# Optimization experiments

Hardware: AMD Instinct MI355X
Metric: run time of the kernel (lower is better)

## Reference

```python
import jax, jax.numpy as jnp
import numpy as np

NUM_E = 50000
EMBED_DIM = 128
HID_DIM = 200
B = 512
N = 50  # candidate_num / history length
ITER_NUM = 3
ALPHA = 0.5
WEIGHT_BASE = 1.0
SQUASH_W = 1.0
SQUASH_EPS = 1e-9
L2_EPS = 1e-12  # torch F.normalize default eps


def setup_inputs() -> dict:
    key = jax.random.key(0)
    k1, k2, k3, k4, k5, k6, k7 = jax.random.split(key, 7)
    idx = jax.random.randint(k1, (B, N), 0, NUM_E)
    times = jax.random.randint(k2, (B, N), 0, 365)
    # embeddings: normal then row-wise L2 normalize (as in init_embeddings)
    emb = jax.random.normal(k3, (NUM_E, EMBED_DIM), dtype=jnp.float32)
    embeddings = emb / jnp.maximum(jnp.linalg.norm(emb, axis=1, keepdims=True), L2_EPS)
    Ws_w = jax.random.normal(k4, (HID_DIM, EMBED_DIM), dtype=jnp.float32) * (2.0 / (HID_DIM + EMBED_DIM)) ** 0.5
    Ws_b = jnp.zeros((HID_DIM,), dtype=jnp.float32)
    mlp_w = jax.random.normal(k5, (NUM_E, HID_DIM), dtype=jnp.float32) * (2.0 / (NUM_E + HID_DIM)) ** 0.5
    mlp_b = jnp.zeros((NUM_E,), dtype=jnp.float32)
    return {"idx": idx, "times": times, "embeddings": embeddings,
            "Ws_w": Ws_w, "Ws_b": Ws_b, "mlp_w": mlp_w, "mlp_b": mlp_b}


def _squash(s):
    # s: [B, H]; squash over last axis (original axis=-2 on [B,1,1,H,1])
    sq = jnp.sum(s * s, axis=-1, keepdims=True)
    scale = sq / (SQUASH_W + sq) / jnp.sqrt(sq + SQUASH_EPS)
    return scale * s


def reference(idx, times, embeddings, Ws_w, Ws_b, mlp_w, mlp_b):
    # gather history embeddings: [B, N, D]
    embeds = embeddings[idx]
    # temporal weighting -> initial routing logits b_ij: [B, N]
    b = (WEIGHT_BASE + 1.0) / (WEIGHT_BASE + times.astype(jnp.float32))
    # Ws linear (dropout is identity at eval): [B, N, H]
    x = jnp.einsum('bnd,hd->bnh', embeds, Ws_w) + Ws_b
    # u_hat: L2-normalized over H
    u_hat = x / jnp.maximum(jnp.linalg.norm(x, axis=-1, keepdims=True), L2_EPS)
    u_det = jax.lax.stop_gradient(u_hat)
    # dynamic routing, fixed ITER_NUM iterations
    for r in range(ITER_NUM):
        c = jax.nn.softmax(b, axis=1) * N            # [B, N]
        s = jnp.einsum('bn,bnh->bh', c, u_hat)       # [B, H]
        v = _squash(s)                               # [B, H]
        if r < ITER_NUM - 1:
            b = b + jnp.einsum('bnh,bh->bn', u_det, v)
    poses, c_ij = v, c                               # [B, H], [B, N]
    # p_ij: scatter-add c_ij per entity id (math of one_hot^T @ c_ij)
    p = jnp.zeros((B, NUM_E), dtype=jnp.float32)
    p = p.at[jnp.arange(B)[:, None], idx].add(c_ij)
    p = jax.nn.softmax(p, axis=1)
    # decoder mlp (reflect=False)
    scores = poses @ mlp_w.T + mlp_b                 # [B, NUM_E]
    sims = jax.nn.softmax(scores, axis=1)
    return jnp.log(ALPHA * p + (1.0 - ALPHA) * sims)
```

## Files before the change

### kernel.cpp

```cpp
#include <hip/hip_runtime.h>
#include <stdint.h>

#define NUM_E 50000
#define EMBED_DIM 128
#define HID_DIM 200
#define BATCH 512
#define NN 50
#define KPAD 224
#define NKT 7
#define NTT2 3136
#define NXB 196
#define PACK_UNITS 784
#define USTRIDE 201
#define EPS 264

typedef short s16x8 __attribute__((ext_vector_type(8)));
typedef float f32x4 __attribute__((ext_vector_type(4)));

__device__ inline unsigned short f2bf(float f) {
  union { float f; unsigned u; } v; v.f = f;
  unsigned r = v.u + 0x7FFF + ((v.u >> 16) & 1);
  return (unsigned short)(r >> 16);
}
__device__ inline float bf2f(unsigned short b) {
  union { unsigned u; float f; } v; v.u = ((unsigned)b) << 16;
  return v.f;
}

__device__ __forceinline__ void gl_lds16(const unsigned short* g, unsigned short* l) {
  __builtin_amdgcn_global_load_lds(
      (const __attribute__((address_space(1))) unsigned int*)g,
      (__attribute__((address_space(3))) unsigned int*)l, 16, 0, 0);
}

__global__ __launch_bounds__(256, 4) void k_score(
    const unsigned short* __restrict__ Ap, const unsigned short* __restrict__ Bp,
    const float* __restrict__ mlp_b, unsigned short* __restrict__ stash,
    float* __restrict__ S_ws)
{
  __shared__ __align__(16) char buf[34816];
  unsigned short (*Bs)[8192] = (unsigned short (*)[8192])buf;
  unsigned short* ep = (unsigned short*)buf;
  float* red = (float*)(buf + 33792);
  const int id = blockIdx.x;
  const int yb = id / 200;
  const int xb = id - yb * 200;
  if (xb >= NXB) return;

  const int tid = threadIdx.x;
  const int w = tid >> 6, lane = tid & 63;
  const int q = lane >> 4, l15 = lane & 15;
  const int mt0 = yb * 4;
  const int m0 = yb * 64;
  const int ntb = xb * 16 + w * 4;

  float bias[4];
  #pragma unroll
  for (int nl = 0; nl < 4; ++nl) {
    const int col = (ntb + nl) * 16 + l15;
    bias[nl] = (col < NUM_E) ? mlp_b[col] : 0.f;
  }
  const unsigned short* apB = Ap + (size_t)mt0 * NKT * 512 + (size_t)lane * 8;
  const unsigned short* bpB = Bp + (size_t)ntb * NKT * 512 + (size_t)lane * 8;

  f32x4 acc[4][4];
  #pragma unroll
  for (int i = 0; i < 4; i++)
    #pragma unroll
    for (int j = 0; j < 4; j++) acc[i][j] = (f32x4){0, 0, 0, 0};

  s16x8 areg[2][4];

  #pragma unroll
  for (int nl = 0; nl < 4; ++nl)
    gl_lds16(bpB + (size_t)nl * NKT * 512, &Bs[0][(w * 4 + nl) * 512]);
  #pragma unroll
  for (int mi = 0; mi < 4; ++mi)
    areg[0][mi] = *(const s16x8*)(apB + (size_t)(mi * NKT) * 512);
  __syncthreads();

  #pragma unroll
  for (int kt = 0; kt < NKT; ++kt) {
    const int cur = kt & 1;
    if (kt < NKT - 1) {
      #pragma unroll
      for (int nl = 0; nl < 4; ++nl)
        gl_lds16(bpB + (size_t)(nl * NKT + kt + 1) * 512,
                 &Bs[cur ^ 1][(w * 4 + nl) * 512]);
      #pragma unroll
      for (int mi = 0; mi < 4; ++mi)
        areg[cur ^ 1][mi] = *(const s16x8*)(apB + (size_t)(mi * NKT + kt + 1) * 512);
    }
    s16x8 bfr[4];
    #pragma unroll
    for (int nl = 0; nl < 4; ++nl)
      bfr[nl] = *(const s16x8*)&Bs[cur][((w * 4 + nl) * 64 + lane) * 8];
    #pragma unroll
    for (int nl = 0; nl < 4; ++nl)
      #pragma unroll
      for (int mi = 0; mi < 4; ++mi)
        acc[mi][nl] = __builtin_amdgcn_mfma_f32_16x16x32_bf16(areg[cur][mi], bfr[nl], acc[mi][nl], 0, 0, 0);
    if (kt < NKT - 1) __syncthreads();
  }

  __syncthreads();

  float rs[4][4];
  #pragma unroll
  for (int mi = 0; mi < 4; mi++)
    #pragma unroll
    for (int p = 0; p < 4; p++) rs[mi][p] = 0.f;
  #pragma unroll
  for (int mi = 0; mi < 4; ++mi)
    #pragma unroll
    for (int nl = 0; nl < 4; ++nl) {
      const int col = (ntb + nl) * 16 + l15;
      const int lc = w * 64 + nl * 16 + l15;
      #pragma unroll
      for (int p = 0; p < 4; p++) {
        const float v = acc[mi][nl][p] + bias[nl];
        const unsigned short vb = f2bf(v);
        ep[(mi * 16 + q * 4 + p) * EPS + lc] = vb;
        if (col < NUM_E) rs[mi][p] += __expf(bf2f(vb));
      }
    }
  #pragma unroll
  for (int m = 1; m < 16; m <<= 1)
    for (int mi = 0; mi < 4; mi++)
      for (int p = 0; p < 4; p++)
        rs[mi][p] += __shfl_xor(rs[mi][p], m, 64);
  if (l15 == 0)
    for (int mi = 0; mi < 4; mi++)
      for (int p = 0; p < 4; p++)
        red[w * 64 + mi * 16 + q * 4 + p] = rs[mi][p];
  __syncthreads();
  if (tid < 64)
    atomicAdd(&S_ws[m0 + tid],
              red[tid] + red[64 + tid] + red[128 + tid] + red[192 + tid]);

  const int xcbase = xb * 256;
  #pragma unroll
  for (int c = tid; c < 2048; c += 256) {
    const int r = c >> 5, c16 = c & 31;
    const int col = xcbase + c16 * 8;
    if (col < NUM_E) {
      const uint4 vv4 = *(const uint4*)&ep[r * EPS + c16 * 8];
      *(uint4*)&stash[(size_t)(m0 + r) * NUM_E + col] = vv4;
    }
  }
}

__global__ __launch_bounds__(256) void k_final(
    const unsigned short* __restrict__ stash,
    const float* __restrict__ D_ws, const float* __restrict__ S_ws,
    float* __restrict__ out)
{
  const int COLS8 = NUM_E / 8;
  const int total = BATCH * COLS8;
  const int stride = gridDim.x * 256;
  for (int u = blockIdx.x * 256 + threadIdx.x; u < total; u += stride) {
    const int b = u / COLS8;
    const int c8 = u - b * COLS8;
    const float invD = 0.5f / D_ws[b];
    const float invS = 0.5f / S_ws[b];
    const size_t base = (size_t)b * NUM_E + (size_t)c8 * 8;
    const uint4 raw = *(const uint4*)(stash + base);
    float o[8];
    const unsigned wds[4] = {raw.x, raw.y, raw.z, raw.w};
    #pragma unroll
    for (int j = 0; j < 4; ++j) {
      const float v0 = bf2f((unsigned short)(wds[j] & 0xFFFF));
      const float v1 = bf2f((unsigned short)(wds[j] >> 16));
      o[2 * j]     = __logf(fmaf(__expf(v0), invS, invD));
      o[2 * j + 1] = __logf(fmaf(__expf(v1), invS, invD));
    }
    *(float4*)(out + base)     = make_float4(o[0], o[1], o[2], o[3]);
    *(float4*)(out + base + 4) = make_float4(o[4], o[5], o[6], o[7]);
  }
}

__global__ __launch_bounds__(256, 3) void k_stage1(
    const int* __restrict__ idx, const int* __restrict__ times,
    const float* __restrict__ emb, const float* __restrict__ Ws_w,
    const float* __restrict__ Ws_b, const float* __restrict__ mlp_w,
    unsigned short* __restrict__ Bp, unsigned short* __restrict__ Ap,
    float* __restrict__ poses_f, float* __restrict__ expa_ws,
    float* __restrict__ D_ws, float* __restrict__ S_ws)
{
  __shared__ __align__(16) char buf[40320];
  __shared__ float cc[NN], bb[NN], vv[HID_DIM], red4[4], scaleS;
  __shared__ int sidx[NN];
  const int u = blockIdx.x;
  const int tid = threadIdx.x;
  const int w = tid >> 6, lane = tid & 63;
  const int q = lane >> 4, l15 = lane & 15;

  if (u < BATCH) {
    const int b = u;
    if (tid < NN) {
      sidx[tid] = idx[b * NN + tid];
      bb[tid] = 2.0f / (1.0f + (float)times[b * NN + tid]);
    }
    __syncthreads();
    unsigned short* Afr = (unsigned short*)buf;
    unsigned short* Bfr = (unsigned short*)(buf + 16384);
    for (int v = tid; v < 1024; v += 256) {
      const int row = v >> 4, c = v & 15;
      const int kt = c >> 2, qq = c & 3;
      unsigned short tmp[8] __attribute__((aligned(16)));
      if (row < NN) {
        const float* src = emb + (size_t)sidx[row] * EMBED_DIM + c * 8;
        float4 f0 = *(const float4*)src;
        float4 f1 = *(const float4*)(src + 4);
        tmp[0] = f2bf(f0.x); tmp[1] = f2bf(f0.y); tmp[2] = f2bf(f0.z); tmp[3] = f2bf(f0.w);
        tmp[4] = f2bf(f1.x); tmp[5] = f2bf(f1.y); tmp[6] = f2bf(f1.z); tmp[7] = f2bf(f1.w);
      } else {
        for (int j = 0; j < 8; j++) tmp[j] = 0;
      }
      *(uint4*)&Afr[(((row >> 4) * 4 + kt) * 64 + qq * 16 + (row & 15)) * 8] = *(uint4*)tmp;
    }
    f32x4 acc[4][4];
    #pragma unroll
    for (int i = 0; i < 4; i++)
      #pragma unroll
      for (int j = 0; j < 4; j++) acc[i][j] = (f32x4){0, 0, 0, 0};
    __syncthreads();
    for (int kt = 0; kt < 4; ++kt) {
      for (int v = tid; v < 832; v += 256) {
        const int n = v >> 2, cq = v & 3;
        unsigned short tmp[8] __attribute__((aligned(16)));
        if (n < HID_DIM) {
          const float* src = Ws_w + (size_t)n * EMBED_DIM + kt * 32 + cq * 8;
          float4 f0 = *(const float4*)src;
          float4 f1 = *(const float4*)(src + 4);
          tmp[0] = f2bf(f0.x); tmp[1] = f2bf(f0.y); tmp[2] = f2bf(f0.z); tmp[3] = f2bf(f0.w);
          tmp[4] = f2bf(f1.x); tmp[5] = f2bf(f1.y); tmp[6] = f2bf(f1.z); tmp[7] = f2bf(f1.w);
        } else {
          for (int j = 0; j < 8; j++) tmp[j] = 0;
        }
        *(uint4*)&Bfr[((n >> 4) * 64 + cq * 16 + (n & 15)) * 8] = *(uint4*)tmp;
      }
      __syncthreads();
      s16x8 a[4];
      #pragma unroll
      for (int mt = 0; mt < 4; ++mt)
        a[mt] = *(const s16x8*)&Afr[((mt * 4 + kt) * 64 + lane) * 8];
      #pragma unroll
      for (int ii = 0; ii < 4; ++ii) {
        const int nt = w + ii * 4;
        if (nt < 13) {
          s16x8 bv = *(const s16x8*)&Bfr[(nt * 64 + lane) * 8];
          #pragma unroll
          for (int mt = 0; mt < 4; ++mt)
            acc[mt][ii] = __builtin_amdgcn_mfma_f32_16x16x32_bf16(a[mt], bv, acc[mt][ii], 0, 0, 0);
        }
      }
      __syncthreads();
    }
    float* uu = (float*)buf;
    #pragma unroll
    for (int ii = 0; ii < 4; ++ii) {
      const int nt = w + ii * 4;
      if (nt < 13) {
        const int col = nt * 16 + l15;
        if (col < HID_DIM) {
          const float bv = Ws_b[col];
          #pragma unroll
          for (int mt = 0; mt < 4; ++mt)
            #pragma unroll
            for (int p = 0; p < 4; p++) {
              const int row = mt * 16 + q * 4 + p;
              if (row < NN) uu[row * USTRIDE + col] = acc[mt][ii][p] + bv;
            }
        }
      }
    }
    __syncthreads();
    const int un = tid >> 2, uc0 = (tid & 3) * 50;
    if (un < NN) {
      float s = 0.f;
      for (int j = 0; j < 50; j++) {
        const float x = uu[un * USTRIDE + uc0 + j];
        s += x * x;
      }
      s += __shfl_xor(s, 1, 64);
      s += __shfl_xor(s, 2, 64);
      const float inv = 1.0f / fmaxf(sqrtf(s), 1e-12f);
      for (int j = 0; j < 50; j++) uu[un * USTRIDE + uc0 + j] *= inv;
    }
    __syncthreads();
    for (int it = 0; it < 3; ++it) {
      if (tid < 64) {
        float x = (tid < NN) ? bb[tid] : -1e30f;
        float m = x;
        for (int d = 1; d < 64; d <<= 1) m = fmaxf(m, __shfl_xor(m, d, 64));
        float e = (tid < NN) ? __expf(x - m) : 0.f;
        float s = e;
        for (int d = 1; d < 64; d <<= 1) s += __shfl_xor(s, d, 64);
        if (tid < NN) cc[tid] = e * (float)NN / s;
      }
      __syncthreads();
      float sh = 0.f;
      if (tid < HID_DIM)
        for (int n = 0; n < NN; n++) sh += cc[n] * uu[n * USTRIDE + tid];
      float sq2 = (tid < HID_DIM) ? sh * sh : 0.f;
      for (int d = 1; d < 64; d <<= 1) sq2 += __shfl_xor(sq2, d, 64);
      if ((tid & 63) == 0) red4[tid >> 6] = sq2;
      __syncthreads();
      if (tid == 0) {
        const float t2 = red4[0] + red4[1] + red4[2] + red4[3];
        scaleS = t2 / (1.0f + t2) / sqrtf(t2 + 1e-9f);
      }
      __syncthreads();
      if (tid < HID_DIM) vv[tid] = scaleS * sh;
      __syncthreads();
      if (it < 2) {
        float d = 0.f;
        if (un < NN)
          for (int j = 0; j < 50; j++)
            d += uu[un * USTRIDE + uc0 + j] * vv[uc0 + j];
        d += __shfl_xor(d, 1, 64);
        d += __shfl_xor(d, 2, 64);
        if (un < NN && (tid & 3) == 0) bb[un] += d;
        __syncthreads();
      }
    }
    if (tid < KPAD) {
      const float val = (tid < HID_DIM) ? vv[tid] : 0.f;
      const int kt = tid >> 5, rem = tid & 31, qq = rem >> 3, j = rem & 7;
      const int mt = b >> 4, ll = b & 15;
      Ap[(size_t)(((mt * NKT + kt) * 64) + qq * 16 + ll) * 8 + j] = f2bf(val);
    }
    if (tid < HID_DIM) poses_f[b * HID_DIM + tid] = vv[tid];
    if (tid < 64) {
      float a2 = 0.f; int first = 1;
      const int my = (tid < NN) ? sidx[tid] : -1;
      if (tid < NN) {
        for (int n = 0; n < NN; n++)
          if (sidx[n] == my) { a2 += cc[n]; if (n < tid) first = 0; }
        expa_ws[b * NN + tid] = __expf(a2);
      }
      float contrib = (tid < NN && first) ? (__expf(a2) - 1.0f) : 0.f;
      for (int d = 1; d < 64; d <<= 1) contrib += __shfl_xor(contrib, d, 64);
      if (tid == 0) D_ws[b] = (float)NUM_E + contrib;
    }
  } else if (u < BATCH + PACK_UNITS) {
    const int pb = u - BATCH;
    unsigned short* smem = (unsigned short*)buf;
    const size_t base_f = (size_t)pb * 64 * HID_DIM;
    const float4* src4 = (const float4*)(mlp_w + base_f);
    for (int i = tid; i < 3200; i += 256) {
      float4 f;
      if (base_f + 4 * (size_t)i + 4 <= (size_t)NUM_E * HID_DIM) f = src4[i];
      else f = make_float4(0.f, 0.f, 0.f, 0.f);
      unsigned short t4[4] __attribute__((aligned(8))) = {
        f2bf(f.x), f2bf(f.y), f2bf(f.z), f2bf(f.w)};
      *(uint2*)&smem[i * 4] = *(uint2*)t4;
    }
    __syncthreads();
    const int nt0 = pb * 4;
    unsigned short* dst = Bp + (size_t)nt0 * NKT * 512;
    for (int s2 = 0; s2 < 7; ++s2) {
      const int fi = s2 * 256 + tid;
      const int fr = fi >> 6;
      const int ln = fi & 63;
      const int nt_l = fr / 7, kt = fr - nt_l * 7;
      const int r = nt_l * 16 + (ln & 15);
      const int kb = kt * 32 + (ln >> 4) * 8;
      uint4 val;
      if (kb < HID_DIM) val = *(const uint4*)&smem[r * HID_DIM + kb];
      else val = make_uint4(0, 0, 0, 0);
      *(uint4*)&dst[(size_t)fi * 8] = val;
    }
  } else {
    S_ws[tid] = 0.f;
    S_ws[256 + tid] = 0.f;
  }
}

__global__ __launch_bounds__(256) void k_fix(
    const int* __restrict__ idx, const float* __restrict__ expa,
    const float* __restrict__ poses_f, const float* __restrict__ mlp_w,
    const float* __restrict__ mlp_b, const float* __restrict__ D_ws,
    const float* __restrict__ S_ws, float* __restrict__ out)
{
  const int t = blockIdx.x * 4 + (threadIdx.x >> 6);
  const int lane = threadIdx.x & 63;
  if (t >= BATCH * NN) return;
  const int b = t / NN;
  const int j = idx[t];
  float dot = 0.f;
  for (int h = lane; h < HID_DIM; h += 64)
    dot += poses_f[b * HID_DIM + h] * mlp_w[(size_t)j * HID_DIM + h];
  for (int m = 1; m < 64; m <<= 1) dot += __shfl_xor(dot, m, 64);
  if (lane == 0) {
    const float s = dot + mlp_b[j];
    out[(size_t)b * NUM_E + j] = __logf(0.5f * expa[t] / D_ws[b] +
                                        0.5f * __expf(s) / S_ws[b]);
  }
}

extern "C" void kernel_launch(void* const* d_in, const int* in_sizes, int n_in,
                              void* d_out, int out_size, void* d_ws, size_t ws_size,
                              hipStream_t stream) {
  const int*   idx   = (const int*)d_in[0];
  const int*   times = (const int*)d_in[1];
  const float* emb   = (const float*)d_in[2];
  const float* Ws_w  = (const float*)d_in[3];
  const float* Ws_b  = (const float*)d_in[4];
  const float* mlp_w = (const float*)d_in[5];
  const float* mlp_b = (const float*)d_in[6];
  float* out = (float*)d_out;

  char* ws = (char*)d_ws;
  unsigned short* Bp    = (unsigned short*)ws; ws += (size_t)NTT2 * NKT * 64 * 8 * 2;
  unsigned short* Ap    = (unsigned short*)ws; ws += (size_t)32 * NKT * 64 * 8 * 2;
  float* poses_f        = (float*)ws;          ws += (size_t)BATCH * HID_DIM * 4;
  float* expa           = (float*)ws;          ws += (size_t)BATCH * NN * 4;
  float* D_ws           = (float*)ws;          ws += (size_t)BATCH * 4;
  float* S_ws           = (float*)ws;          ws += (size_t)BATCH * 4;
  unsigned short* stash = (unsigned short*)ws; ws += (size_t)BATCH * NUM_E * 2;

  k_stage1 <<<dim3(BATCH + PACK_UNITS + 1), 256, 0, stream>>>(
      idx, times, emb, Ws_w, Ws_b, mlp_w, Bp, Ap, poses_f, expa, D_ws, S_ws);
  k_score  <<<dim3(1600), 256, 0, stream>>>(Ap, Bp, mlp_b, stash, S_ws);
  k_final  <<<dim3(2048), 256, 0, stream>>>(stash, D_ws, S_ws, out);
  k_fix    <<<dim3(BATCH * NN / 4), 256, 0, stream>>>(idx, expa, poses_f, mlp_w, mlp_b, D_ws, S_ws, out);
}
```

Measured before the change: 255.9 us.

## Fuse score GEMM and final log-mix into one persistent kernel with grid barrier

Merges k_score and k_final into a single kernel launched with 784 blocks. Each block computes two 64-row score tiles and stashes only one of them. After a software grid barrier that makes the row softmax sums complete, it writes the final log output straight from LDS for the tile it kept and from the stash for the other. This removes one launch and roughly halves the bf16 stash write and read-back traffic. The cost is spin-wait synchronisation, which relies on all 784 blocks being co-resident (4 per CU at 256 CUs) and would deadlock otherwise.

```diff
diff --git a/kernel.cpp b/kernel.cpp
--- a/kernel.cpp
+++ b/kernel.cpp
@@ -13,6 +13,8 @@
 #define PACK_UNITS 784
 #define USTRIDE 201
 #define EPS 264
+#define NBAR 196
+#define GRID_SF 784
 
 typedef short s16x8 __attribute__((ext_vector_type(8)));
 typedef float f32x4 __attribute__((ext_vector_type(4)));
@@ -33,25 +35,25 @@
       (__attribute__((address_space(3))) unsigned int*)l, 16, 0, 0);
 }
 
-__global__ __launch_bounds__(256, 4) void k_score(
+__global__ __launch_bounds__(256, 4) void k_scoref(
     const unsigned short* __restrict__ Ap, const unsigned short* __restrict__ Bp,
     const float* __restrict__ mlp_b, unsigned short* __restrict__ stash,
-    float* __restrict__ S_ws)
+    float* __restrict__ S_ws, const float* __restrict__ D_ws,
+    unsigned int* __restrict__ bar, float* __restrict__ out)
 {
   __shared__ __align__(16) char buf[34816];
   unsigned short (*Bs)[8192] = (unsigned short (*)[8192])buf;
   unsigned short* ep = (unsigned short*)buf;
   float* red = (float*)(buf + 33792);
-  const int id = blockIdx.x;
-  const int yb = id / 200;
-  const int xb = id - yb * 200;
-  if (xb >= NXB) return;
+
+  const int b = blockIdx.x;
+  const int xb = b % NXB;
+  const int ybN = b / NXB;
+  const int ybF = ybN + 4;
 
   const int tid = threadIdx.x;
   const int w = tid >> 6, lane = tid & 63;
   const int q = lane >> 4, l15 = lane & 15;
-  const int mt0 = yb * 4;
-  const int m0 = yb * 64;
   const int ntb = xb * 16 + w * 4;
 
   float bias[4];
@@ -60,122 +62,163 @@
     const int col = (ntb + nl) * 16 + l15;
     bias[nl] = (col < NUM_E) ? mlp_b[col] : 0.f;
   }
-  const unsigned short* apB = Ap + (size_t)mt0 * NKT * 512 + (size_t)lane * 8;
   const unsigned short* bpB = Bp + (size_t)ntb * NKT * 512 + (size_t)lane * 8;
 
-  f32x4 acc[4][4];
-  #pragma unroll
-  for (int i = 0; i < 4; i++)
-    #pragma unroll
-    for (int j = 0; j < 4; j++) acc[i][j] = (f32x4){0, 0, 0, 0};
-
-  s16x8 areg[2][4];
-
-  #pragma unroll
-  for (int nl = 0; nl < 4; ++nl)
-    gl_lds16(bpB + (size_t)nl * NKT * 512, &Bs[0][(w * 4 + nl) * 512]);
-  #pragma unroll
-  for (int mi = 0; mi < 4; ++mi)
-    areg[0][mi] = *(const s16x8*)(apB + (size_t)(mi * NKT) * 512);
+  for (int t = 0; t < 2; ++t) {
+    const int yb = (t == 0) ? ybF : ybN;
+    const int m0 = yb * 64;
+    const unsigned short* apB = Ap + (size_t)(yb * 4) * NKT * 512 + (size_t)lane * 8;
+
+    f32x4 acc[4][4];
+    #pragma unroll
+    for (int i = 0; i < 4; i++)
+      #pragma unroll
+      for (int j = 0; j < 4; j++) acc[i][j] = (f32x4){0, 0, 0, 0};
+
+    s16x8 areg[2][4];
+    __syncthreads();
+    #pragma unroll
+    for (int nl = 0; nl < 4; ++nl)
+      gl_lds16(bpB + (size_t)nl * NKT * 512, &Bs[0][(w * 4 + nl) * 512]);
+    #pragma unroll
+    for (int mi = 0; mi < 4; ++mi)
+      areg[0][mi] = *(const s16x8*)(apB + (size_t)(mi * NKT) * 512);
+    __syncthreads();
+
+    #pragma unroll
+    for (int kt = 0; kt < NKT; ++kt) {
+      const int cur = kt & 1;
+      if (kt < NKT - 1) {
+        #pragma unroll
+        for (int nl = 0; nl < 4; ++nl)
+          gl_lds16(bpB + (size_t)(nl * NKT + kt + 1) * 512,
+                   &Bs[cur ^ 1][(w * 4 + nl) * 512]);
+        #pragma unroll
+        for (int mi = 0; mi < 4; ++mi)
+          areg[cur ^ 1][mi] = *(const s16x8*)(apB + (size_t)(mi * NKT + kt + 1) * 512);
+      }
+      s16x8 bfr[4];
+      #pragma unroll
+      for (int nl = 0; nl < 4; ++nl)
+        bfr[nl] = *(const s16x8*)&Bs[cur][((w * 4 + nl) * 64 + lane) * 8];
+      #pragma unroll
+      for (int nl = 0; nl < 4; ++nl)
+        #pragma unroll
+        for (int mi = 0; mi < 4; ++mi)
+          acc[mi][nl] = __builtin_amdgcn_mfma_f32_16x16x32_bf16(areg[cur][mi], bfr[nl], acc[mi][nl], 0, 0, 0);
+      if (kt < NKT - 1) __syncthreads();
+    }
+    __syncthreads();
+
+    float rs[4][4];
+    #pragma unroll
+    for (int mi = 0; mi < 4; mi++)
+      #pragma unroll
+      for (int p = 0; p < 4; p++) rs[mi][p] = 0.f;
+    #pragma unroll
+    for (int mi = 0; mi < 4; ++mi)
+      #pragma unroll
+      for (int nl = 0; nl < 4; ++nl) {
+        const int col = (ntb + nl) * 16 + l15;
+        const int lc = w * 64 + nl * 16 + l15;
+        #pragma unroll
+        for (int p = 0; p < 4; p++) {
+          const float v = acc[mi][nl][p] + bias[nl];
+          const unsigned short vb = f2bf(v);
+          ep[(mi * 16 + q * 4 + p) * EPS + lc] = vb;
+          if (col < NUM_E) rs[mi][p] += __expf(bf2f(vb));
+        }
+      }
+    #pragma unroll
+    for (int m = 1; m < 16; m <<= 1)
+      for (int mi = 0; mi < 4; mi++)
+        for (int p = 0; p < 4; p++)
+          rs[mi][p] += __shfl_xor(rs[mi][p], m, 64);
+    if (l15 == 0)
+      for (int mi = 0; mi < 4; mi++)
+        for (int p = 0; p < 4; p++)
+          red[w * 64 + mi * 16 + q * 4 + p] = rs[mi][p];
+    __syncthreads();
+    if (tid < 64)
+      atomicAdd(&S_ws[m0 + tid],
+                red[tid] + red[64 + tid] + red[128 + tid] + red[192 + tid]);
+
+    if (t == 0) {
+      const int xcbase = xb * 256;
+      #pragma unroll
+      for (int c = tid; c < 2048; c += 256) {
+        const int r = c >> 5, ch = c & 31;
+        const int col = xcbase + ch * 8;
+        if (col < NUM_E) {
+          const uint4 vv4 = *(const uint4*)&ep[r * EPS + ch * 8];
+          *(uint4*)&stash[(size_t)(m0 + r) * NUM_E + col] = vv4;
+        }
+      }
+    }
+  }
+
   __syncthreads();
-
-  #pragma unroll
-  for (int kt = 0; kt < NKT; ++kt) {
-    const int cur = kt & 1;
-    if (kt < NKT - 1) {
-      #pragma unroll
-      for (int nl = 0; nl < 4; ++nl)
-        gl_lds16(bpB + (size_t)(nl * NKT + kt + 1) * 512,
-                 &Bs[cur ^ 1][(w * 4 + nl) * 512]);
-      #pragma unroll
-      for (int mi = 0; mi < 4; ++mi)
-        areg[cur ^ 1][mi] = *(const s16x8*)(apB + (size_t)(mi * NKT + kt + 1) * 512);
-    }
-    s16x8 bfr[4];
-    #pragma unroll
-    for (int nl = 0; nl < 4; ++nl)
-      bfr[nl] = *(const s16x8*)&Bs[cur][((w * 4 + nl) * 64 + lane) * 8];
-    #pragma unroll
-    for (int nl = 0; nl < 4; ++nl)
-      #pragma unroll
-      for (int mi = 0; mi < 4; ++mi)
-        acc[mi][nl] = __builtin_amdgcn_mfma_f32_16x16x32_bf16(areg[cur][mi], bfr[nl], acc[mi][nl], 0, 0, 0);
-    if (kt < NKT - 1) __syncthreads();
-  }
-
+  __threadfence();
+  if (tid == 0) {
+    __hip_atomic_fetch_add(bar, 1u, __ATOMIC_ACQ_REL, __HIP_MEMORY_SCOPE_AGENT);
+    while (__hip_atomic_load(bar, __ATOMIC_ACQUIRE, __HIP_MEMORY_SCOPE_AGENT) < GRID_SF)
+      __builtin_amdgcn_s_sleep(8);
+  }
   __syncthreads();
 
-  float rs[4][4];
-  #pragma unroll
-  for (int mi = 0; mi < 4; mi++)
-    #pragma unroll
-    for (int p = 0; p < 4; p++) rs[mi][p] = 0.f;
-  #pragma unroll
-  for (int mi = 0; mi < 4; ++mi)
-    #pragma unroll
-    for (int nl = 0; nl < 4; ++nl) {
-      const int col = (ntb + nl) * 16 + l15;
-      const int lc = w * 64 + nl * 16 + l15;
-      #pragma unroll
-      for (int p = 0; p < 4; p++) {
-        const float v = acc[mi][nl][p] + bias[nl];
-        const unsigned short vb = f2bf(v);
-        ep[(mi * 16 + q * 4 + p) * EPS + lc] = vb;
-        if (col < NUM_E) rs[mi][p] += __expf(bf2f(vb));
-      }
-    }
-  #pragma unroll
-  for (int m = 1; m < 16; m <<= 1)
-    for (int mi = 0; mi < 4; mi++)
-      for (int p = 0; p < 4; p++)
-        rs[mi][p] += __shfl_xor(rs[mi][p], m, 64);
-  if (l15 == 0)
-    for (int mi = 0; mi < 4; mi++)
-      for (int p = 0; p < 4; p++)
-        red[w * 64 + mi * 16 + q * 4 + p] = rs[mi][p];
+  const int m0N = ybN * 64, m0F = ybF * 64;
+  if (tid < 64) {
+    const float sN = atomicAdd(&S_ws[m0N + tid], 0.0f);
+    const float sF = atomicAdd(&S_ws[m0F + tid], 0.0f);
+    red[tid]       = 0.5f / D_ws[m0N + tid];
+    red[64 + tid]  = 0.5f / sN;
+    red[128 + tid] = 0.5f / D_ws[m0F + tid];
+    red[192 + tid] = 0.5f / sF;
+  }
   __syncthreads();
-  if (tid < 64)
-    atomicAdd(&S_ws[m0 + tid],
-              red[tid] + red[64 + tid] + red[128 + tid] + red[192 + tid]);
 
   const int xcbase = xb * 256;
   #pragma unroll
   for (int c = tid; c < 2048; c += 256) {
-    const int r = c >> 5, c16 = c & 31;
-    const int col = xcbase + c16 * 8;
+    const int r = c >> 5, ch = c & 31;
+    const int col = xcbase + ch * 8;
     if (col < NUM_E) {
-      const uint4 vv4 = *(const uint4*)&ep[r * EPS + c16 * 8];
-      *(uint4*)&stash[(size_t)(m0 + r) * NUM_E + col] = vv4;
-    }
-  }
-}
-
-__global__ __launch_bounds__(256) void k_final(
-    const unsigned short* __restrict__ stash,
-    const float* __restrict__ D_ws, const float* __restrict__ S_ws,
-    float* __restrict__ out)
-{
-  const int COLS8 = NUM_E / 8;
-  const int total = BATCH * COLS8;
-  const int stride = gridDim.x * 256;
-  for (int u = blockIdx.x * 256 + threadIdx.x; u < total; u += stride) {
-    const int b = u / COLS8;
-    const int c8 = u - b * COLS8;
-    const float invD = 0.5f / D_ws[b];
-    const float invS = 0.5f / S_ws[b];
-    const size_t base = (size_t)b * NUM_E + (size_t)c8 * 8;
-    const uint4 raw = *(const uint4*)(stash + base);
-    float o[8];
-    const unsigned wds[4] = {raw.x, raw.y, raw.z, raw.w};
-    #pragma unroll
-    for (int j = 0; j < 4; ++j) {
-      const float v0 = bf2f((unsigned short)(wds[j] & 0xFFFF));
-      const float v1 = bf2f((unsigned short)(wds[j] >> 16));
-      o[2 * j]     = __logf(fmaf(__expf(v0), invS, invD));
-      o[2 * j + 1] = __logf(fmaf(__expf(v1), invS, invD));
-    }
-    *(float4*)(out + base)     = make_float4(o[0], o[1], o[2], o[3]);
-    *(float4*)(out + base + 4) = make_float4(o[4], o[5], o[6], o[7]);
+      const uint4 raw = *(const uint4*)&ep[r * EPS + ch * 8];
+      const float invD = red[r], invS = red[64 + r];
+      const unsigned wds[4] = {raw.x, raw.y, raw.z, raw.w};
+      float o[8];
+      #pragma unroll
+      for (int j = 0; j < 4; ++j) {
+        const float v0 = bf2f((unsigned short)(wds[j] & 0xFFFF));
+        const float v1 = bf2f((unsigned short)(wds[j] >> 16));
+        o[2 * j]     = __logf(fmaf(__expf(v0), invS, invD));
+        o[2 * j + 1] = __logf(fmaf(__expf(v1), invS, invD));
+      }
+      const size_t base = (size_t)(m0N + r) * NUM_E + col;
+      *(float4*)&out[base]     = make_float4(o[0], o[1], o[2], o[3]);
+      *(float4*)&out[base + 4] = make_float4(o[4], o[5], o[6], o[7]);
+    }
+  }
+  #pragma unroll
+  for (int c = tid; c < 2048; c += 256) {
+    const int r = c >> 5, ch = c & 31;
+    const int col = xcbase + ch * 8;
+    if (col < NUM_E) {
+      const uint4 raw = *(const uint4*)&stash[(size_t)(m0F + r) * NUM_E + col];
+      const float invD = red[128 + r], invS = red[192 + r];
+      const unsigned wds[4] = {raw.x, raw.y, raw.z, raw.w};
+      float o[8];
+      #pragma unroll
+      for (int j = 0; j < 4; ++j) {
+        const float v0 = bf2f((unsigned short)(wds[j] & 0xFFFF));
+        const float v1 = bf2f((unsigned short)(wds[j] >> 16));
+        o[2 * j]     = __logf(fmaf(__expf(v0), invS, invD));
+        o[2 * j + 1] = __logf(fmaf(__expf(v1), invS, invD));
+      }
+      const size_t base = (size_t)(m0F + r) * NUM_E + col;
+      *(float4*)&out[base]     = make_float4(o[0], o[1], o[2], o[3]);
+      *(float4*)&out[base + 4] = make_float4(o[4], o[5], o[6], o[7]);
+    }
   }
 }
 
@@ -185,7 +228,8 @@
     const float* __restrict__ Ws_b, const float* __restrict__ mlp_w,
     unsigned short* __restrict__ Bp, unsigned short* __restrict__ Ap,
     float* __restrict__ poses_f, float* __restrict__ expa_ws,
-    float* __restrict__ D_ws, float* __restrict__ S_ws)
+    float* __restrict__ D_ws, float* __restrict__ S_ws,
+    unsigned int* __restrict__ bar)
 {
   __shared__ __align__(16) char buf[40320];
   __shared__ float cc[NN], bb[NN], vv[HID_DIM], red4[4], scaleS;
@@ -375,6 +419,7 @@
   } else {
     S_ws[tid] = 0.f;
     S_ws[256 + tid] = 0.f;
+    if (tid == 0) bar[0] = 0u;
   }
 }
 
@@ -419,11 +464,11 @@
   float* expa           = (float*)ws;          ws += (size_t)BATCH * NN * 4;
   float* D_ws           = (float*)ws;          ws += (size_t)BATCH * 4;
   float* S_ws           = (float*)ws;          ws += (size_t)BATCH * 4;
+  unsigned int* bar     = (unsigned int*)ws;   ws += 16;
   unsigned short* stash = (unsigned short*)ws; ws += (size_t)BATCH * NUM_E * 2;
 
   k_stage1 <<<dim3(BATCH + PACK_UNITS + 1), 256, 0, stream>>>(
-      idx, times, emb, Ws_w, Ws_b, mlp_w, Bp, Ap, poses_f, expa, D_ws, S_ws);
-  k_score  <<<dim3(1600), 256, 0, stream>>>(Ap, Bp, mlp_b, stash, S_ws);
-  k_final  <<<dim3(2048), 256, 0, stream>>>(stash, D_ws, S_ws, out);
+      idx, times, emb, Ws_w, Ws_b, mlp_w, Bp, Ap, poses_f, expa, D_ws, S_ws, bar);
+  k_scoref <<<dim3(GRID_SF), 256, 0, stream>>>(Ap, Bp, mlp_b, stash, S_ws, D_ws, bar, out);
   k_fix    <<<dim3(BATCH * NN / 4), 256, 0, stream>>>(idx, expa, poses_f, mlp_w, mlp_b, D_ws, S_ws, out);
 }
```

Measured after the change: 463.0 us. 80.9% more time.
